# Kernel optimization log

Hardware: AMD Instinct MI355X
Metric: run time of the kernel (lower is better)

The kernel has to match this reference:

```python
import jax, jax.numpy as jnp
import numpy as np

H = 2048
NCLS = 11

def setup_inputs() -> dict:
    key = jax.random.key(0)
    ks = jax.random.split(key, 8)
    s = 1.0 / np.sqrt(H)
    return {
        "inputs": jax.random.normal(ks[0], (512, H), dtype=jnp.float32),
        "W_ih": jax.random.uniform(ks[1], (4 * H, H), jnp.float32, -s, s),
        "W_hh": jax.random.uniform(ks[2], (4 * H, H), jnp.float32, -s, s),
        "b_ih": jax.random.uniform(ks[3], (4 * H,), jnp.float32, -s, s),
        "b_hh": jax.random.uniform(ks[4], (4 * H,), jnp.float32, -s, s),
        "W_out": jax.random.uniform(ks[5], (NCLS, H), jnp.float32, -s, s),
        "b_out": jax.random.uniform(ks[6], (NCLS,), jnp.float32, -s, s),
        "steps": 512,
    }

def reference(inputs, W_ih, W_hh, b_ih, b_hh, W_out, b_out, steps):
    # previous step's output (hidden state) is fed back as the next input.
    # PyTorch LSTM gate order: i, f, g, o.
    def cell(carry, _):
        x, h, c = carry  # each (1, H)
        gates = x @ W_ih.T + b_ih + h @ W_hh.T + b_hh  # (1, 4H)
        i, f, g, o = jnp.split(gates, 4, axis=-1)
        i = jax.nn.sigmoid(i)
        f = jax.nn.sigmoid(f)
        g = jnp.tanh(g)
        o = jax.nn.sigmoid(o)
        c = f * c + i * g
        h = o * jnp.tanh(c)
        # output (= h) becomes next step's input
        return (h, h, c), None

    x0 = inputs[0:1]  # (1, H)
    h0 = jnp.zeros((1, H), inputs.dtype)
    c0 = jnp.zeros((1, H), inputs.dtype)
    (_, h, c), _ = jax.lax.scan(cell, (x0, h0, c0), None, length=steps)

    logits = h @ W_out.T + b_out           # (1, 11)
    probs = jax.nn.softmax(logits, axis=-1)
    return probs, h, c
```

## Files before the change

kernel.cpp:

```cpp
#include <hip/hip_runtime.h>
#include <cstdint>
#include <cstddef>

#define HDIM 2048
#define NCLS 11
#define NBLK 256
#define NTHR 256
#define EPB  (HDIM / NBLK)
#define CHUNK 256
#define CPAD  260


__device__ __forceinline__ float waveReduceSum(float v) {
#pragma unroll
    for (int off = 32; off > 0; off >>= 1) v += __shfl_xor(v, off, 64);
    return v;
}

__global__ void __launch_bounds__(NTHR, 1) lstm_persistent(
    const float* __restrict__ x0,
    const float* __restrict__ Wih,
    const float* __restrict__ Whh,
    const float* __restrict__ bih,
    const float* __restrict__ bhh,
    const float* __restrict__ Wout,
    const float* __restrict__ bout,
    const int* __restrict__ stepsp,
    float* __restrict__ out,
    float* __restrict__ tag0,
    float* __restrict__ tag1,
    int sw)
{
    const int tid  = threadIdx.x;
    const int wave = tid >> 6;
    const int lane = tid & 63;
    const int rl   = lane >> 3;
    const int cc   = lane & 7;
    const int bid  = blockIdx.x;
    const int jb   = bid * EPB;

    __shared__ float hlds[8 * CPAD];
    __shared__ float gsm[4 * EPB];
    __shared__ float csm[EPB];

    const int row = wave * HDIM + jb + rl;
    const size_t sbase = (size_t)row * HDIM + (size_t)cc * CHUNK;

    float w[CHUNK];
#pragma unroll
    for (int jj = 0; jj < 64; ++jj) {
        float4 v = *(const float4*)(Wih + sbase + (size_t)jj * 4);
        w[4 * jj + 0] = v.x; w[4 * jj + 1] = v.y;
        w[4 * jj + 2] = v.z; w[4 * jj + 3] = v.w;
    }
    const float bsum = bih[row] + bhh[row];
    if (tid < EPB) csm[tid] = 0.0f;

    const int steps = stepsp[0];
    const int e0   = tid * 8;
    const int soff = (tid >> 5) * CPAD + (tid & 31) * 8;

    for (int t = 0; t < steps; ++t) {
        if (t == 0) {
#pragma unroll
            for (int i = 0; i < 8; ++i) hlds[soff + i] = x0[e0 + i];
        } else {
            float* tb   = (t & 1) ? tag1 : tag0;
            float* slot = tb + (size_t)tid * sw;
            unsigned* genp = (unsigned*)(slot + 8);
            while (__hip_atomic_load(genp, __ATOMIC_RELAXED, __HIP_MEMORY_SCOPE_AGENT)
                   < (unsigned)t)
                __builtin_amdgcn_s_sleep(1);
            asm volatile("" ::: "memory");
#pragma unroll
            for (int i = 0; i < 8; ++i)
                hlds[soff + i] = __hip_atomic_load(slot + i, __ATOMIC_RELAXED,
                                                   __HIP_MEMORY_SCOPE_AGENT);
        }
        __syncthreads();

        const float* hc = &hlds[cc * CPAD];
        float ax = 0.f, ay = 0.f, az = 0.f, aw = 0.f;
#pragma unroll
        for (int jj = 0; jj < 64; ++jj) {
            float4 hv = *(const float4*)(hc + jj * 4);
            ax += w[4 * jj + 0] * hv.x;
            ay += w[4 * jj + 1] * hv.y;
            az += w[4 * jj + 2] * hv.z;
            aw += w[4 * jj + 3] * hv.w;
        }
        float part = (ax + ay) + (az + aw);
        part += __shfl_xor(part, 1, 64);
        part += __shfl_xor(part, 2, 64);
        part += __shfl_xor(part, 4, 64);
        if (cc == 0) gsm[wave * EPB + rl] = part + bsum;
        __syncthreads();

        float* wbuf = ((t + 1) & 1) ? tag1 : tag0;
        float* wslot = wbuf + (size_t)bid * sw;
        if (tid < EPB) {
            float gi = gsm[0 * EPB + tid];
            float gf = gsm[1 * EPB + tid];
            float gg = gsm[2 * EPB + tid];
            float go = gsm[3 * EPB + tid];
            float si = 1.0f / (1.0f + expf(-gi));
            float sf = 1.0f / (1.0f + expf(-gf));
            float tg = tanhf(gg);
            float so = 1.0f / (1.0f + expf(-go));
            float c  = sf * csm[tid] + si * tg;
            csm[tid] = c;
            __hip_atomic_store(wslot + tid, so * tanhf(c),
                               __ATOMIC_RELAXED, __HIP_MEMORY_SCOPE_AGENT);
        }
        __syncthreads();
        if (tid == 0)
            __hip_atomic_store((unsigned*)(wslot + 8), (unsigned)(t + 1),
                               __ATOMIC_RELAXED, __HIP_MEMORY_SCOPE_AGENT);

        if (t == 0) {
#pragma unroll
            for (int jj = 0; jj < 64; ++jj) {
                float4 v = *(const float4*)(Whh + sbase + (size_t)jj * 4);
                w[4 * jj + 0] += v.x; w[4 * jj + 1] += v.y;
                w[4 * jj + 2] += v.z; w[4 * jj + 3] += v.w;
            }
        }
    }

    if (tid < EPB) out[NCLS + HDIM + jb + tid] = csm[tid];

    if (bid == 0) {
        float* tb   = (steps & 1) ? tag1 : tag0;
        float* slot = tb + (size_t)tid * sw;
        unsigned* genp = (unsigned*)(slot + 8);
        while (__hip_atomic_load(genp, __ATOMIC_RELAXED, __HIP_MEMORY_SCOPE_AGENT)
               < (unsigned)steps)
            __builtin_amdgcn_s_sleep(1);
        asm volatile("" ::: "memory");
#pragma unroll
        for (int i = 0; i < 8; ++i)
            hlds[soff + i] = __hip_atomic_load(slot + i, __ATOMIC_RELAXED,
                                               __HIP_MEMORY_SCOPE_AGENT);
        __syncthreads();

        __shared__ float lsm[NCLS];
        float hr[8][4];
#pragma unroll
        for (int k = 0; k < 8; ++k)
#pragma unroll
            for (int c = 0; c < 4; ++c)
                hr[k][c] = hlds[k * CPAD + lane * 4 + c];
        for (int r = wave; r < NCLS; r += 4) {
            const float4* w4 = (const float4*)(Wout + (size_t)r * HDIM);
            float sx = 0.f, sy = 0.f, sz = 0.f, sw4 = 0.f;
#pragma unroll
            for (int k = 0; k < 8; ++k) {
                float4 wv = w4[k * 64 + lane];
                sx  += wv.x * hr[k][0];
                sy  += wv.y * hr[k][1];
                sz  += wv.z * hr[k][2];
                sw4 += wv.w * hr[k][3];
            }
            float s = waveReduceSum((sx + sy) + (sz + sw4));
            if (lane == 0) lsm[r] = s + bout[r];
        }
        __syncthreads();
        if (tid == 0) {
            float m = lsm[0];
            for (int r = 1; r < NCLS; ++r) m = fmaxf(m, lsm[r]);
            float ex[NCLS];
            float den = 0.0f;
            for (int r = 0; r < NCLS; ++r) { ex[r] = expf(lsm[r] - m); den += ex[r]; }
            float inv = 1.0f / den;
            for (int r = 0; r < NCLS; ++r) out[r] = ex[r] * inv;
        }
#pragma unroll
        for (int i = 0; i < 8; ++i)
            out[NCLS + e0 + i] = hlds[soff + i];
    }
}

extern "C" void kernel_launch(void* const* d_in, const int* in_sizes, int n_in,
                              void* d_out, int out_size, void* d_ws, size_t ws_size,
                              hipStream_t stream) {
    const float* x0    = (const float*)d_in[0];
    const float* Wih   = (const float*)d_in[1];
    const float* Whh   = (const float*)d_in[2];
    const float* bih   = (const float*)d_in[3];
    const float* bhh   = (const float*)d_in[4];
    const float* Wout  = (const float*)d_in[5];
    const float* bout  = (const float*)d_in[6];
    const int*   steps = (const int*)d_in[7];
    float* out = (float*)d_out;

    int sw = 16;
    size_t need = (size_t)2 * NBLK * sw * sizeof(float);
    if (ws_size < need) { sw = 9; need = (size_t)2 * NBLK * sw * sizeof(float); }

    float* tag0 = (float*)d_ws;
    float* tag1 = tag0 + (size_t)NBLK * sw;

    hipMemsetAsync(d_ws, 0, need, stream);

    lstm_persistent<<<dim3(NBLK), dim3(NTHR), 0, stream>>>(
        x0, Wih, Whh, bih, bhh, Wout, bout, steps, out, tag0, tag1, sw);
}
```

Baseline: 2.997 ms.

## Pack step tag with hidden value and compute gates in-wave without block barriers

```diff
diff --git a/kernel.cpp b/kernel.cpp
--- a/kernel.cpp
+++ b/kernel.cpp
@@ -6,7 +6,6 @@
 #define NCLS 11
 #define NBLK 256
 #define NTHR 256
-#define EPB  (HDIM / NBLK)
 #define CHUNK 256
 #define CPAD  260
 
@@ -27,23 +26,23 @@
     const float* __restrict__ bout,
     const int* __restrict__ stepsp,
     float* __restrict__ out,
-    float* __restrict__ tag0,
-    float* __restrict__ tag1,
-    int sw)
+    unsigned long long* __restrict__ pairs0,
+    unsigned long long* __restrict__ pairs1)
 {
     const int tid  = threadIdx.x;
     const int wave = tid >> 6;
     const int lane = tid & 63;
     const int rl   = lane >> 3;
     const int cc   = lane & 7;
+    const int gate = rl & 3;
+    const int eloc = rl >> 2;
     const int bid  = blockIdx.x;
-    const int jb   = bid * EPB;
-
-    __shared__ float hlds[8 * CPAD];
-    __shared__ float gsm[4 * EPB];
-    __shared__ float csm[EPB];
-
-    const int row = wave * HDIM + jb + rl;
+    const int jb   = bid * 8;
+    const int elem = jb + 2 * wave + eloc;
+
+    __shared__ float hlds[2][8 * CPAD];
+
+    const int row = gate * HDIM + elem;
     const size_t sbase = (size_t)row * HDIM + (size_t)cc * CHUNK;
 
     float w[CHUNK];
@@ -54,32 +53,48 @@
         w[4 * jj + 2] = v.z; w[4 * jj + 3] = v.w;
     }
     const float bsum = bih[row] + bhh[row];
-    if (tid < EPB) csm[tid] = 0.0f;
+    float creg = 0.0f, hreg = 0.0f;
 
     const int steps = stepsp[0];
     const int e0   = tid * 8;
     const int soff = (tid >> 5) * CPAD + (tid & 31) * 8;
 
     for (int t = 0; t < steps; ++t) {
+        const int p = t & 1;
         if (t == 0) {
-#pragma unroll
-            for (int i = 0; i < 8; ++i) hlds[soff + i] = x0[e0 + i];
+            float4 a = *(const float4*)(x0 + e0);
+            float4 b = *(const float4*)(x0 + e0 + 4);
+            *(float4*)&hlds[0][soff]     = a;
+            *(float4*)&hlds[0][soff + 4] = b;
         } else {
-            float* tb   = (t & 1) ? tag1 : tag0;
-            float* slot = tb + (size_t)tid * sw;
-            unsigned* genp = (unsigned*)(slot + 8);
-            while (__hip_atomic_load(genp, __ATOMIC_RELAXED, __HIP_MEMORY_SCOPE_AGENT)
-                   < (unsigned)t)
+            const unsigned long long* pp = (p ? pairs1 : pairs0) + e0;
+            unsigned long long pv[8];
+            for (;;) {
+                bool ready = true;
+#pragma unroll
+                for (int i = 0; i < 8; ++i) {
+                    pv[i] = __hip_atomic_load(pp + i, __ATOMIC_RELAXED,
+                                              __HIP_MEMORY_SCOPE_AGENT);
+                    ready &= ((unsigned)(pv[i] >> 32) == (unsigned)t);
+                }
+                if (ready) break;
                 __builtin_amdgcn_s_sleep(1);
-            asm volatile("" ::: "memory");
-#pragma unroll
-            for (int i = 0; i < 8; ++i)
-                hlds[soff + i] = __hip_atomic_load(slot + i, __ATOMIC_RELAXED,
-                                                   __HIP_MEMORY_SCOPE_AGENT);
-        }
-        __syncthreads();
-
-        const float* hc = &hlds[cc * CPAD];
+            }
+            float4 a, b;
+            a.x = __uint_as_float((unsigned)pv[0]);
+            a.y = __uint_as_float((unsigned)pv[1]);
+            a.z = __uint_as_float((unsigned)pv[2]);
+            a.w = __uint_as_float((unsigned)pv[3]);
+            b.x = __uint_as_float((unsigned)pv[4]);
+            b.y = __uint_as_float((unsigned)pv[5]);
+            b.z = __uint_as_float((unsigned)pv[6]);
+            b.w = __uint_as_float((unsigned)pv[7]);
+            *(float4*)&hlds[p][soff]     = a;
+            *(float4*)&hlds[p][soff + 4] = b;
+        }
+        __syncthreads();
+
+        const float* hc = &hlds[p][cc * CPAD];
         float ax = 0.f, ay = 0.f, az = 0.f, aw = 0.f;
 #pragma unroll
         for (int jj = 0; jj < 64; ++jj) {
@@ -93,29 +108,28 @@
         part += __shfl_xor(part, 1, 64);
         part += __shfl_xor(part, 2, 64);
         part += __shfl_xor(part, 4, 64);
-        if (cc == 0) gsm[wave * EPB + rl] = part + bsum;
-        __syncthreads();
-
-        float* wbuf = ((t + 1) & 1) ? tag1 : tag0;
-        float* wslot = wbuf + (size_t)bid * sw;
-        if (tid < EPB) {
-            float gi = gsm[0 * EPB + tid];
-            float gf = gsm[1 * EPB + tid];
-            float gg = gsm[2 * EPB + tid];
-            float go = gsm[3 * EPB + tid];
-            float si = 1.0f / (1.0f + expf(-gi));
-            float sf = 1.0f / (1.0f + expf(-gf));
-            float tg = tanhf(gg);
-            float so = 1.0f / (1.0f + expf(-go));
-            float c  = sf * csm[tid] + si * tg;
-            csm[tid] = c;
-            __hip_atomic_store(wslot + tid, so * tanhf(c),
+        part += bsum;
+
+        const int sb = (lane & 0x20) | (lane & 7);
+        float gi = __shfl(part, sb + 0,  64);
+        float gf = __shfl(part, sb + 8,  64);
+        float gg = __shfl(part, sb + 16, 64);
+        float go = __shfl(part, sb + 24, 64);
+
+        float si = 1.0f / (1.0f + expf(-gi));
+        float sf = 1.0f / (1.0f + expf(-gf));
+        float tg = tanhf(gg);
+        float so = 1.0f / (1.0f + expf(-go));
+        creg = sf * creg + si * tg;
+        hreg = so * tanhf(creg);
+
+        if ((lane & 31) == 0) {
+            unsigned long long pk =
+                ((unsigned long long)(unsigned)(t + 1) << 32) |
+                (unsigned long long)__float_as_uint(hreg);
+            __hip_atomic_store((((t + 1) & 1) ? pairs1 : pairs0) + elem, pk,
                                __ATOMIC_RELAXED, __HIP_MEMORY_SCOPE_AGENT);
         }
-        __syncthreads();
-        if (tid == 0)
-            __hip_atomic_store((unsigned*)(wslot + 8), (unsigned)(t + 1),
-                               __ATOMIC_RELAXED, __HIP_MEMORY_SCOPE_AGENT);
 
         if (t == 0) {
 #pragma unroll
@@ -127,20 +141,30 @@
         }
     }
 
-    if (tid < EPB) out[NCLS + HDIM + jb + tid] = csm[tid];
+    if ((lane & 31) == 0) {
+        out[NCLS + elem]        = hreg;
+        out[NCLS + HDIM + elem] = creg;
+    }
 
     if (bid == 0) {
-        float* tb   = (steps & 1) ? tag1 : tag0;
-        float* slot = tb + (size_t)tid * sw;
-        unsigned* genp = (unsigned*)(slot + 8);
-        while (__hip_atomic_load(genp, __ATOMIC_RELAXED, __HIP_MEMORY_SCOPE_AGENT)
-               < (unsigned)steps)
+        __syncthreads();
+        const unsigned long long* pp =
+            ((steps & 1) ? pairs1 : pairs0) + e0;
+        unsigned long long pv[8];
+        for (;;) {
+            bool ready = true;
+#pragma unroll
+            for (int i = 0; i < 8; ++i) {
+                pv[i] = __hip_atomic_load(pp + i, __ATOMIC_RELAXED,
+                                          __HIP_MEMORY_SCOPE_AGENT);
+                ready &= ((unsigned)(pv[i] >> 32) == (unsigned)steps);
+            }
+            if (ready) break;
             __builtin_amdgcn_s_sleep(1);
-        asm volatile("" ::: "memory");
+        }
 #pragma unroll
         for (int i = 0; i < 8; ++i)
-            hlds[soff + i] = __hip_atomic_load(slot + i, __ATOMIC_RELAXED,
-                                               __HIP_MEMORY_SCOPE_AGENT);
+            hlds[0][soff + i] = __uint_as_float((unsigned)pv[i]);
         __syncthreads();
 
         __shared__ float lsm[NCLS];
@@ -149,7 +173,7 @@
         for (int k = 0; k < 8; ++k)
 #pragma unroll
             for (int c = 0; c < 4; ++c)
-                hr[k][c] = hlds[k * CPAD + lane * 4 + c];
+                hr[k][c] = hlds[0][k * CPAD + lane * 4 + c];
         for (int r = wave; r < NCLS; r += 4) {
             const float4* w4 = (const float4*)(Wout + (size_t)r * HDIM);
             float sx = 0.f, sy = 0.f, sz = 0.f, sw4 = 0.f;
@@ -174,9 +198,6 @@
             float inv = 1.0f / den;
             for (int r = 0; r < NCLS; ++r) out[r] = ex[r] * inv;
         }
-#pragma unroll
-        for (int i = 0; i < 8; ++i)
-            out[NCLS + e0 + i] = hlds[soff + i];
     }
 }
 
@@ -193,15 +214,12 @@
     const int*   steps = (const int*)d_in[7];
     float* out = (float*)d_out;
 
-    int sw = 16;
-    size_t need = (size_t)2 * NBLK * sw * sizeof(float);
-    if (ws_size < need) { sw = 9; need = (size_t)2 * NBLK * sw * sizeof(float); }
-
-    float* tag0 = (float*)d_ws;
-    float* tag1 = tag0 + (size_t)NBLK * sw;
-
-    hipMemsetAsync(d_ws, 0, need, stream);
+    unsigned long long* pairs0 = (unsigned long long*)d_ws;
+    unsigned long long* pairs1 = pairs0 + HDIM;
+
+    hipMemsetAsync(d_ws, 0, (size_t)2 * HDIM * sizeof(unsigned long long),
+                   stream);
 
     lstm_persistent<<<dim3(NBLK), dim3(NTHR), 0, stream>>>(
-        x0, Wih, Whh, bih, bhh, Wout, bout, steps, out, tag0, tag1, sw);
+        x0, Wih, Whh, bih, bhh, Wout, bout, steps, out, pairs0, pairs1);
 }
```

Measured after the change: 4.423 ms. 47.6% more time.

## Embed step tag in low mantissa bits of published hidden values, cut block syncs

Applied to the files above, without the earlier changes.

```diff
diff --git a/kernel.cpp b/kernel.cpp
--- a/kernel.cpp
+++ b/kernel.cpp
@@ -4,18 +4,11 @@
 
 #define HDIM 2048
 #define NCLS 11
-#define NBLK 256
-#define NTHR 256
-#define EPB  (HDIM / NBLK)
-#define CHUNK 256
-#define CPAD  260
-
-
-__device__ __forceinline__ float waveReduceSum(float v) {
-#pragma unroll
-    for (int off = 32; off > 0; off >>= 1) v += __shfl_xor(v, off, 64);
-    return v;
-}
+#define NBLK 128
+#define NTHR 512
+#define NPAIR (HDIM / 2)
+#define LSZ 2304
+
 
 __global__ void __launch_bounds__(NTHR, 1) lstm_persistent(
     const float* __restrict__ x0,
@@ -27,141 +20,183 @@
     const float* __restrict__ bout,
     const int* __restrict__ stepsp,
     float* __restrict__ out,
-    float* __restrict__ tag0,
-    float* __restrict__ tag1,
-    int sw)
+    unsigned long long* __restrict__ hpub0,
+    unsigned long long* __restrict__ hpub1)
 {
     const int tid  = threadIdx.x;
     const int wave = tid >> 6;
     const int lane = tid & 63;
-    const int rl   = lane >> 3;
-    const int cc   = lane & 7;
     const int bid  = blockIdx.x;
-    const int jb   = bid * EPB;
-
-    __shared__ float hlds[8 * CPAD];
-    __shared__ float gsm[4 * EPB];
-    __shared__ float csm[EPB];
-
-    const int row = wave * HDIM + jb + rl;
-    const size_t sbase = (size_t)row * HDIM + (size_t)cc * CHUNK;
-
-    float w[CHUNK];
-#pragma unroll
-    for (int jj = 0; jj < 64; ++jj) {
-        float4 v = *(const float4*)(Wih + sbase + (size_t)jj * 4);
-        w[4 * jj + 0] = v.x; w[4 * jj + 1] = v.y;
-        w[4 * jj + 2] = v.z; w[4 * jj + 3] = v.w;
-    }
-    const float bsum = bih[row] + bhh[row];
-    if (tid < EPB) csm[tid] = 0.0f;
+    const int e0   = bid * 16 + 2 * wave;
+
+    __shared__ float hlds[2][LSZ];
+    __shared__ float lsm[NCLS];
+
+    float4 w4[8][8];
+#pragma unroll
+    for (int r = 0; r < 8; ++r) {
+        const int R = (r & 3) * HDIM + e0 + (r >> 2);
+        const float* src = Wih + (size_t)R * HDIM + 32 * lane;
+#pragma unroll
+        for (int k = 0; k < 8; ++k) w4[r][k] = *(const float4*)(src + 4 * k);
+    }
+    float bs[8];
+#pragma unroll
+    for (int r = 0; r < 8; ++r) {
+        const int R = (r & 3) * HDIM + e0 + (r >> 2);
+        bs[r] = bih[R] + bhh[R];
+    }
+    float creg0 = 0.f, creg1 = 0.f, hreg0 = 0.f, hreg1 = 0.f;
 
     const int steps = stepsp[0];
-    const int e0   = tid * 8;
-    const int soff = (tid >> 5) * CPAD + (tid & 31) * 8;
+    const int o0 = 2 * tid + 4 * ((2 * tid) >> 5);
+    const int o1 = 2 * (tid + NTHR) + 4 * ((2 * (tid + NTHR)) >> 5);
 
     for (int t = 0; t < steps; ++t) {
+        const int p = t & 1;
         if (t == 0) {
-#pragma unroll
-            for (int i = 0; i < 8; ++i) hlds[soff + i] = x0[e0 + i];
+            *(float2*)&hlds[0][o0] = *(const float2*)(x0 + 2 * tid);
+            *(float2*)&hlds[0][o1] = *(const float2*)(x0 + 2 * (tid + NTHR));
         } else {
-            float* tb   = (t & 1) ? tag1 : tag0;
-            float* slot = tb + (size_t)tid * sw;
-            unsigned* genp = (unsigned*)(slot + 8);
-            while (__hip_atomic_load(genp, __ATOMIC_RELAXED, __HIP_MEMORY_SCOPE_AGENT)
-                   < (unsigned)t)
+            const unsigned exp8 = ((unsigned)t >> 1) & 0xFFu;
+            const unsigned long long* hp = p ? hpub1 : hpub0;
+            unsigned long long v0 = __hip_atomic_load(hp + tid,
+                __ATOMIC_RELAXED, __HIP_MEMORY_SCOPE_AGENT);
+            unsigned long long v1 = __hip_atomic_load(hp + tid + NTHR,
+                __ATOMIC_RELAXED, __HIP_MEMORY_SCOPE_AGENT);
+            for (;;) {
+                const bool r0 = (((unsigned)v0 & 0xFFu) == exp8) &&
+                                (((unsigned)(v0 >> 32) & 0xFFu) == exp8);
+                const bool r1 = (((unsigned)v1 & 0xFFu) == exp8) &&
+                                (((unsigned)(v1 >> 32) & 0xFFu) == exp8);
+                if (r0 && r1) break;
                 __builtin_amdgcn_s_sleep(1);
-            asm volatile("" ::: "memory");
-#pragma unroll
-            for (int i = 0; i < 8; ++i)
-                hlds[soff + i] = __hip_atomic_load(slot + i, __ATOMIC_RELAXED,
-                                                   __HIP_MEMORY_SCOPE_AGENT);
+                if (!r0) v0 = __hip_atomic_load(hp + tid,
+                    __ATOMIC_RELAXED, __HIP_MEMORY_SCOPE_AGENT);
+                if (!r1) v1 = __hip_atomic_load(hp + tid + NTHR,
+                    __ATOMIC_RELAXED, __HIP_MEMORY_SCOPE_AGENT);
+            }
+            float2 s0, s1;
+            s0.x = __uint_as_float((unsigned)v0 & 0xFFFFFF00u);
+            s0.y = __uint_as_float((unsigned)(v0 >> 32) & 0xFFFFFF00u);
+            s1.x = __uint_as_float((unsigned)v1 & 0xFFFFFF00u);
+            s1.y = __uint_as_float((unsigned)(v1 >> 32) & 0xFFFFFF00u);
+            *(float2*)&hlds[p][o0] = s0;
+            *(float2*)&hlds[p][o1] = s1;
         }
         __syncthreads();
 
-        const float* hc = &hlds[cc * CPAD];
-        float ax = 0.f, ay = 0.f, az = 0.f, aw = 0.f;
-#pragma unroll
-        for (int jj = 0; jj < 64; ++jj) {
-            float4 hv = *(const float4*)(hc + jj * 4);
-            ax += w[4 * jj + 0] * hv.x;
-            ay += w[4 * jj + 1] * hv.y;
-            az += w[4 * jj + 2] * hv.z;
-            aw += w[4 * jj + 3] * hv.w;
-        }
-        float part = (ax + ay) + (az + aw);
-        part += __shfl_xor(part, 1, 64);
-        part += __shfl_xor(part, 2, 64);
-        part += __shfl_xor(part, 4, 64);
-        if (cc == 0) gsm[wave * EPB + rl] = part + bsum;
+        const float* hc = &hlds[p][36 * lane];
+        float acc[8];
+#pragma unroll
+        for (int r = 0; r < 8; ++r) acc[r] = 0.f;
+#pragma unroll
+        for (int k = 0; k < 8; ++k) {
+            const float4 hv = *(const float4*)(hc + 4 * k);
+#pragma unroll
+            for (int r = 0; r < 8; ++r) {
+                acc[r] += w4[r][k].x * hv.x + w4[r][k].y * hv.y
+                        + w4[r][k].z * hv.z + w4[r][k].w * hv.w;
+            }
+        }
+#pragma unroll
+        for (int s = 1; s < 64; s <<= 1)
+#pragma unroll
+            for (int r = 0; r < 8; ++r)
+                acc[r] += __shfl_xor(acc[r], s, 64);
+
+        {
+            const float gi = acc[0] + bs[0], gf = acc[1] + bs[1];
+            const float gg = acc[2] + bs[2], go = acc[3] + bs[3];
+            const float si = 1.0f / (1.0f + expf(-gi));
+            const float sf = 1.0f / (1.0f + expf(-gf));
+            const float so = 1.0f / (1.0f + expf(-go));
+            creg0 = sf * creg0 + si * tanhf(gg);
+            hreg0 = so * tanhf(creg0);
+        }
+        {
+            const float gi = acc[4] + bs[4], gf = acc[5] + bs[5];
+            const float gg = acc[6] + bs[6], go = acc[7] + bs[7];
+            const float si = 1.0f / (1.0f + expf(-gi));
+            const float sf = 1.0f / (1.0f + expf(-gf));
+            const float so = 1.0f / (1.0f + expf(-go));
+            creg1 = sf * creg1 + si * tanhf(gg);
+            hreg1 = so * tanhf(creg1);
+        }
+
+        if (lane == 0) {
+            const unsigned t8 = ((unsigned)(t + 1) >> 1) & 0xFFu;
+            const unsigned u0 = ((__float_as_uint(hreg0) + 0x80u) & 0xFFFFFF00u) | t8;
+            const unsigned u1 = ((__float_as_uint(hreg1) + 0x80u) & 0xFFFFFF00u) | t8;
+            const unsigned long long pk =
+                ((unsigned long long)u1 << 32) | (unsigned long long)u0;
+            __hip_atomic_store((((t + 1) & 1) ? hpub1 : hpub0) + (bid * 8 + wave),
+                               pk, __ATOMIC_RELAXED, __HIP_MEMORY_SCOPE_AGENT);
+        }
+
+        if (t == 0) {
+#pragma unroll
+            for (int r = 0; r < 8; ++r) {
+                const int R = (r & 3) * HDIM + e0 + (r >> 2);
+                const float* src = Whh + (size_t)R * HDIM + 32 * lane;
+#pragma unroll
+                for (int k = 0; k < 8; ++k) {
+                    const float4 v = *(const float4*)(src + 4 * k);
+                    w4[r][k].x += v.x; w4[r][k].y += v.y;
+                    w4[r][k].z += v.z; w4[r][k].w += v.w;
+                }
+            }
+        }
+    }
+
+    if (lane == 0) {
+        out[NCLS + e0]            = hreg0;
+        out[NCLS + e0 + 1]        = hreg1;
+        out[NCLS + HDIM + e0]     = creg0;
+        out[NCLS + HDIM + e0 + 1] = creg1;
+    }
+
+    if (bid == 0) {
+        const int sp = steps & 1;
+        const unsigned exp8 = ((unsigned)steps >> 1) & 0xFFu;
+        const unsigned long long* hp = sp ? hpub1 : hpub0;
+        unsigned long long v0 = __hip_atomic_load(hp + tid,
+            __ATOMIC_RELAXED, __HIP_MEMORY_SCOPE_AGENT);
+        unsigned long long v1 = __hip_atomic_load(hp + tid + NTHR,
+            __ATOMIC_RELAXED, __HIP_MEMORY_SCOPE_AGENT);
+        for (;;) {
+            const bool r0 = (((unsigned)v0 & 0xFFu) == exp8) &&
+                            (((unsigned)(v0 >> 32) & 0xFFu) == exp8);
+            const bool r1 = (((unsigned)v1 & 0xFFu) == exp8) &&
+                            (((unsigned)(v1 >> 32) & 0xFFu) == exp8);
+            if (r0 && r1) break;
+            __builtin_amdgcn_s_sleep(1);
+            if (!r0) v0 = __hip_atomic_load(hp + tid,
+                __ATOMIC_RELAXED, __HIP_MEMORY_SCOPE_AGENT);
+            if (!r1) v1 = __hip_atomic_load(hp + tid + NTHR,
+                __ATOMIC_RELAXED, __HIP_MEMORY_SCOPE_AGENT);
+        }
+        hlds[sp][o0]     = __uint_as_float((unsigned)v0 & 0xFFFFFF00u);
+        hlds[sp][o0 + 1] = __uint_as_float((unsigned)(v0 >> 32) & 0xFFFFFF00u);
+        hlds[sp][o1]     = __uint_as_float((unsigned)v1 & 0xFFFFFF00u);
+        hlds[sp][o1 + 1] = __uint_as_float((unsigned)(v1 >> 32) & 0xFFFFFF00u);
         __syncthreads();
 
-        float* wbuf = ((t + 1) & 1) ? tag1 : tag0;
-        float* wslot = wbuf + (size_t)bid * sw;
-        if (tid < EPB) {
-            float gi = gsm[0 * EPB + tid];
-            float gf = gsm[1 * EPB + tid];
-            float gg = gsm[2 * EPB + tid];
-            float go = gsm[3 * EPB + tid];
-            float si = 1.0f / (1.0f + expf(-gi));
-            float sf = 1.0f / (1.0f + expf(-gf));
-            float tg = tanhf(gg);
-            float so = 1.0f / (1.0f + expf(-go));
-            float c  = sf * csm[tid] + si * tg;
-            csm[tid] = c;
-            __hip_atomic_store(wslot + tid, so * tanhf(c),
-                               __ATOMIC_RELAXED, __HIP_MEMORY_SCOPE_AGENT);
-        }
-        __syncthreads();
-        if (tid == 0)
-            __hip_atomic_store((unsigned*)(wslot + 8), (unsigned)(t + 1),
-                               __ATOMIC_RELAXED, __HIP_MEMORY_SCOPE_AGENT);
-
-        if (t == 0) {
-#pragma unroll
-            for (int jj = 0; jj < 64; ++jj) {
-                float4 v = *(const float4*)(Whh + sbase + (size_t)jj * 4);
-                w[4 * jj + 0] += v.x; w[4 * jj + 1] += v.y;
-                w[4 * jj + 2] += v.z; w[4 * jj + 3] += v.w;
-            }
-        }
-    }
-
-    if (tid < EPB) out[NCLS + HDIM + jb + tid] = csm[tid];
-
-    if (bid == 0) {
-        float* tb   = (steps & 1) ? tag1 : tag0;
-        float* slot = tb + (size_t)tid * sw;
-        unsigned* genp = (unsigned*)(slot + 8);
-        while (__hip_atomic_load(genp, __ATOMIC_RELAXED, __HIP_MEMORY_SCOPE_AGENT)
-               < (unsigned)steps)
-            __builtin_amdgcn_s_sleep(1);
-        asm volatile("" ::: "memory");
-#pragma unroll
-        for (int i = 0; i < 8; ++i)
-            hlds[soff + i] = __hip_atomic_load(slot + i, __ATOMIC_RELAXED,
-                                               __HIP_MEMORY_SCOPE_AGENT);
-        __syncthreads();
-
-        __shared__ float lsm[NCLS];
-        float hr[8][4];
-#pragma unroll
-        for (int k = 0; k < 8; ++k)
-#pragma unroll
-            for (int c = 0; c < 4; ++c)
-                hr[k][c] = hlds[k * CPAD + lane * 4 + c];
-        for (int r = wave; r < NCLS; r += 4) {
-            const float4* w4 = (const float4*)(Wout + (size_t)r * HDIM);
-            float sx = 0.f, sy = 0.f, sz = 0.f, sw4 = 0.f;
+        const float* hc = &hlds[sp][36 * lane];
+        float4 hv[8];
+#pragma unroll
+        for (int k = 0; k < 8; ++k) hv[k] = *(const float4*)(hc + 4 * k);
+        for (int r = wave; r < NCLS; r += 8) {
+            const float* wr = Wout + (size_t)r * HDIM + 32 * lane;
+            float s = 0.f;
 #pragma unroll
             for (int k = 0; k < 8; ++k) {
-                float4 wv = w4[k * 64 + lane];
-                sx  += wv.x * hr[k][0];
-                sy  += wv.y * hr[k][1];
-                sz  += wv.z * hr[k][2];
-                sw4 += wv.w * hr[k][3];
-            }
-            float s = waveReduceSum((sx + sy) + (sz + sw4));
+                const float4 wv = *(const float4*)(wr + 4 * k);
+                s += wv.x * hv[k].x + wv.y * hv[k].y
+                   + wv.z * hv[k].z + wv.w * hv[k].w;
+            }
+#pragma unroll
+            for (int st = 1; st < 64; st <<= 1) s += __shfl_xor(s, st, 64);
             if (lane == 0) lsm[r] = s + bout[r];
         }
         __syncthreads();
@@ -171,12 +206,9 @@
             float ex[NCLS];
             float den = 0.0f;
             for (int r = 0; r < NCLS; ++r) { ex[r] = expf(lsm[r] - m); den += ex[r]; }
-            float inv = 1.0f / den;
+            const float inv = 1.0f / den;
             for (int r = 0; r < NCLS; ++r) out[r] = ex[r] * inv;
         }
-#pragma unroll
-        for (int i = 0; i < 8; ++i)
-            out[NCLS + e0 + i] = hlds[soff + i];
     }
 }
 
@@ -193,15 +225,12 @@
     const int*   steps = (const int*)d_in[7];
     float* out = (float*)d_out;
 
-    int sw = 16;
-    size_t need = (size_t)2 * NBLK * sw * sizeof(float);
-    if (ws_size < need) { sw = 9; need = (size_t)2 * NBLK * sw * sizeof(float); }
-
-    float* tag0 = (float*)d_ws;
-    float* tag1 = tag0 + (size_t)NBLK * sw;
-
-    hipMemsetAsync(d_ws, 0, need, stream);
+    unsigned long long* hpub0 = (unsigned long long*)d_ws;
+    unsigned long long* hpub1 = hpub0 + NPAIR;
+
+    hipMemsetAsync(d_ws, 0xFF, (size_t)2 * NPAIR * sizeof(unsigned long long),
+                   stream);
 
     lstm_persistent<<<dim3(NBLK), dim3(NTHR), 0, stream>>>(
-        x0, Wih, Whh, bih, bhh, Wout, bout, steps, out, tag0, tag1, sw);
+        x0, Wih, Whh, bih, bhh, Wout, bout, steps, out, hpub0, hpub1);
 }
```

After: 5.340 ms. 1.78x slower.
